# Optimization experiments

Hardware: AMD Instinct MI355X
Metric: run time of the kernel (lower is better)

## Reference

```python
import jax, jax.numpy as jnp
import numpy as np

NUM_HEADS = 16
DIM = 1024
HD = DIM // NUM_HEADS  # 64


def setup_inputs() -> dict:
    key = jax.random.key(0)
    ks = jax.random.split(key, 7)
    B, S = 4, 2048
    def xavier(k, shape, fan_in, fan_out):
        bound = float(np.sqrt(6.0 / (fan_in + fan_out)))
        return jax.random.uniform(k, shape, jnp.float32, -bound, bound)
    return {
        "q": jax.random.normal(ks[0], (B, S, DIM), jnp.float32),
        "k": jax.random.normal(ks[1], (B, S, DIM), jnp.float32),
        "v": jax.random.normal(ks[2], (B, S, DIM), jnp.float32),
        "Wq": xavier(ks[3], (NUM_HEADS, DIM, HD), DIM, HD),
        "Wk": xavier(ks[4], (NUM_HEADS, DIM, HD), DIM, HD),
        "Wv": xavier(ks[5], (NUM_HEADS, DIM, HD), DIM, HD),
        "Wo": xavier(ks[6], (DIM, DIM), DIM, DIM),
    }


def reference(q, k, v, Wq, Wk, Wv, Wo):
    B, S, D = q.shape
    norm = jnp.sqrt(jnp.asarray(HD, q.dtype))
    # per-head projections: [B,S,D] x [H,D,hd] -> [B,H,S,hd]
    qh = jnp.einsum('bsd,hde->bhse', q, Wq)
    kh = jnp.einsum('bsd,hde->bhse', k, Wk)
    vh = jnp.einsum('bsd,hde->bhse', v, Wv)
    # scores [B,H,S,S]
    scores = jnp.einsum('bhse,bhte->bhst', qh, kh) / norm
    causal = jnp.triu(jnp.ones((S, S), bool), k=1)
    scores = jnp.where(causal, -jnp.inf, scores)
    attn = jax.nn.softmax(scores, axis=-1)
    out = jnp.einsum('bhst,bhte->bhse', attn, vh)  # [B,H,S,hd]
    # faithful to original: a raw view of [B,H,S,hd] -> [B,S,H*hd] (no head transpose)
    out = out.reshape(B, S, NUM_HEADS * HD)
    return jnp.matmul(out, Wo)
```

## Files before the change

### kernel.cpp

```cpp
#include <hip/hip_runtime.h>
#include <hip/hip_bf16.h>
#include <stdint.h>

typedef __bf16 bf16;
typedef __bf16 bf16x8 __attribute__((ext_vector_type(8)));
typedef __bf16 bf16x4 __attribute__((ext_vector_type(4)));
typedef __bf16 bf16x2 __attribute__((ext_vector_type(2)));
typedef float f32x4 __attribute__((ext_vector_type(4)));
typedef float f32x16 __attribute__((ext_vector_type(16)));
typedef int i32x4 __attribute__((ext_vector_type(4)));

#define NH   16
#define SEQ  2048
#define DM   1024
#define HD   64

__device__ __forceinline__ int swz(int r, int o) {
  return o ^ ((r & 7) << 4) ^ (((r >> 3) & 1) << 5);
}

__device__ __forceinline__ int tauK(int m) {
  return (m & ~12) | ((m & 4) << 1) | ((m & 8) >> 1);
}

__device__ __forceinline__ void gll16(const void* g, void* l) {
  __builtin_amdgcn_global_load_lds(
      (__attribute__((address_space(1))) unsigned int*)(g),
      (__attribute__((address_space(3))) unsigned int*)(l), 16, 0, 0);
}

__device__ __forceinline__ int pk2(float a, float b) {
  bf16x2 t; t[0] = (bf16)a; t[1] = (bf16)b;
  return __builtin_bit_cast(int, t);
}

__global__ __launch_bounds__(256) void conv_wt(const float* __restrict__ Wq,
                                               const float* __restrict__ Wk,
                                               const float* __restrict__ Wv,
                                               const float* __restrict__ Wo,
                                               bf16* __restrict__ WqT,
                                               bf16* __restrict__ WkT,
                                               bf16* __restrict__ WvT,
                                               bf16* __restrict__ WoT) {
  __shared__ float tile[64][65];
  int z = blockIdx.z, t = threadIdx.x;
  int d0 = blockIdx.x << 6;
  if (z < 3) {
    const float* W = (z == 0 ? Wq : z == 1 ? Wk : Wv) + ((size_t)blockIdx.y << 16);
#pragma unroll
    for (int i = 0; i < 4; ++i) {
      int slot = (i << 8) + t;
      int r = slot >> 4, c4 = (slot & 15) << 2;
      float4 fv = *(const float4*)(W + (size_t)(d0 + r) * 64 + c4);
      tile[r][c4] = fv.x; tile[r][c4 + 1] = fv.y;
      tile[r][c4 + 2] = fv.z; tile[r][c4 + 3] = fv.w;
    }
  } else {
    int n0 = blockIdx.y << 6;
#pragma unroll
    for (int i = 0; i < 4; ++i) {
      int slot = (i << 8) + t;
      int r = slot >> 4, c4 = (slot & 15) << 2;
      float4 fv = *(const float4*)(Wo + (size_t)(d0 + r) * 1024 + n0 + c4);
      tile[r][c4] = fv.x; tile[r][c4 + 1] = fv.y;
      tile[r][c4 + 2] = fv.z; tile[r][c4 + 3] = fv.w;
    }
  }
  __syncthreads();
  bf16* Wt = z == 0 ? WqT : z == 1 ? WkT : z == 2 ? WvT : WoT;
  size_t base = (z < 3) ? ((size_t)blockIdx.y << 16)
                        : (size_t)(blockIdx.y << 6) * 1024;
  int e = t >> 2, dq = (t & 3) << 4;
  bf16x8 o0, o1;
#pragma unroll
  for (int j = 0; j < 8; ++j) {
    o0[j] = (bf16)tile[dq + j][e];
    o1[j] = (bf16)tile[dq + 8 + j][e];
  }
  bf16* p = Wt + base + (size_t)e * 1024 + d0 + dq;
  *(bf16x8*)p = o0;
  *(bf16x8*)(p + 8) = o1;
}

__global__ __launch_bounds__(256) void conv_in(const float* __restrict__ q,
                                               const float* __restrict__ k,
                                               const float* __restrict__ v,
                                               bf16* __restrict__ qb,
                                               bf16* __restrict__ kb,
                                               bf16* __restrict__ vb) {
  int z = blockIdx.y;
  const float* src = z == 0 ? q : z == 1 ? k : v;
  bf16* dst = z == 0 ? qb : z == 1 ? kb : vb;
  int i = (blockIdx.x * 256 + threadIdx.x) << 4;
  float4 f0 = *(const float4*)(src + i);
  float4 f1 = *(const float4*)(src + i + 4);
  float4 f2 = *(const float4*)(src + i + 8);
  float4 f3 = *(const float4*)(src + i + 12);
  bf16x8 o0, o1;
  o0[0] = (bf16)f0.x; o0[1] = (bf16)f0.y; o0[2] = (bf16)f0.z; o0[3] = (bf16)f0.w;
  o0[4] = (bf16)f1.x; o0[5] = (bf16)f1.y; o0[6] = (bf16)f1.z; o0[7] = (bf16)f1.w;
  o1[0] = (bf16)f2.x; o1[1] = (bf16)f2.y; o1[2] = (bf16)f2.z; o1[3] = (bf16)f2.w;
  o1[4] = (bf16)f3.x; o1[5] = (bf16)f3.y; o1[6] = (bf16)f3.z; o1[7] = (bf16)f3.w;
  *(bf16x8*)(dst + i) = o0;
  *(bf16x8*)(dst + i + 8) = o1;
}

template <bool AF32>
__device__ __forceinline__ void gemm_body(char* sm, const void* Av,
                                          const bf16* Bt, void* Cv, int epi,
                                          float scale, int n0, int m0) {
  char* As = sm;
  char* Bs = sm + 16384;
  int tid = threadIdx.x;
  int wid = tid >> 6, lane = tid & 63;
  int g = lane >> 4, cc = lane & 15;
  int wr = wid >> 1, wc = wid & 1;

  f32x4 acc[4][4];
#pragma unroll
  for (int a = 0; a < 4; ++a)
#pragma unroll
    for (int b = 0; b < 4; ++b)
#pragma unroll
      for (int j = 0; j < 4; ++j) acc[a][b][j] = 0.0f;

  for (int kt = 0; kt < 16; ++kt) {
    int k0 = kt << 6;
#pragma unroll
    for (int it = 0; it < 4; ++it) {
      int L = (it << 12) + (tid << 4);
      int r = L >> 7, o = L & 127;
      int os = swz(r, o);
      gll16(Bt + (size_t)(n0 + r) * 1024 + k0 + (os >> 1),
            Bs + (it << 12) + (wid << 10));
    }
    if constexpr (AF32) {
      const float* A = (const float*)Av;
      int r = tid >> 1, hf = tid & 1;
      const float* src = A + (size_t)(m0 + r) * 1024 + k0 + hf * 32;
      float4 fv[8];
#pragma unroll
      for (int q = 0; q < 8; ++q) fv[q] = ((const float4*)src)[q];
#pragma unroll
      for (int q = 0; q < 4; ++q) {
        float4 a = fv[2 * q], b = fv[2 * q + 1];
        bf16x8 pk;
        pk[0] = (bf16)a.x; pk[1] = (bf16)a.y; pk[2] = (bf16)a.z; pk[3] = (bf16)a.w;
        pk[4] = (bf16)b.x; pk[5] = (bf16)b.y; pk[6] = (bf16)b.z; pk[7] = (bf16)b.w;
        *(bf16x8*)(As + (r << 7) + swz(r, hf * 64 + q * 16)) = pk;
      }
    } else {
      const bf16* A = (const bf16*)Av;
#pragma unroll
      for (int it = 0; it < 4; ++it) {
        int L = (it << 12) + (tid << 4);
        int r = L >> 7, o = L & 127;
        int os = swz(r, o);
        gll16(A + (size_t)(m0 + r) * 1024 + k0 + (os >> 1),
              As + (it << 12) + (wid << 10));
      }
    }
    __syncthreads();
#pragma unroll
    for (int kk = 0; kk < 2; ++kk) {
      bf16x8 af[4], bfr[4];
#pragma unroll
      for (int fm = 0; fm < 4; ++fm) {
        int r = (wr << 6) + (fm << 4) + cc;
        af[fm] = *(const bf16x8*)(As + (r << 7) + swz(r, (kk << 6) + (g << 4)));
      }
#pragma unroll
      for (int fn = 0; fn < 4; ++fn) {
        int r = (wc << 6) + (fn << 4) + cc;
        bfr[fn] = *(const bf16x8*)(Bs + (r << 7) + swz(r, (kk << 6) + (g << 4)));
      }
#pragma unroll
      for (int fm = 0; fm < 4; ++fm)
#pragma unroll
        for (int fn = 0; fn < 4; ++fn)
          acc[fm][fn] = __builtin_amdgcn_mfma_f32_16x16x32_bf16(
              af[fm], bfr[fn], acc[fm][fn], 0, 0, 0);
    }
    __syncthreads();
  }

#pragma unroll
  for (int fm = 0; fm < 4; ++fm) {
#pragma unroll
    for (int fn = 0; fn < 4; ++fn) {
      f32x4 v = acc[fm][fn];
      int mr = m0 + (wr << 6) + (fm << 4) + (g << 2);
      int n = n0 + (wc << 6) + (fn << 4) + cc;
      if (epi == 2) {
        float* C = (float*)Cv;
#pragma unroll
        for (int j = 0; j < 4; ++j) C[(size_t)(mr + j) * 1024 + n] = v[j];
      } else if (epi == 0) {
        bf16* C = (bf16*)Cv;
        int h = n >> 6, e = n & 63;
#pragma unroll
        for (int j = 0; j < 4; ++j) {
          int b = (mr + j) >> 11, s = (mr + j) & 2047;
          C[((size_t)(b * NH + h) * SEQ + s) * HD + e] = (bf16)(v[j] * scale);
        }
      } else {
        bf16* C = (bf16*)Cv;
        int h = n >> 6, e = n & 63;
        int b = mr >> 11, s = mr & 2047;
        bf16x4 t;
#pragma unroll
        for (int j = 0; j < 4; ++j) t[j] = (bf16)v[j];
        *(bf16x4*)(C + ((size_t)(b * NH + h) * HD + e) * SEQ + s) = t;
      }
    }
  }
}

__global__ __launch_bounds__(256, 4) void gemm_qkv_bf16(
    const bf16* __restrict__ qb, const bf16* __restrict__ kb,
    const bf16* __restrict__ vb, const bf16* __restrict__ Wq,
    const bf16* __restrict__ Wk, const bf16* __restrict__ Wv,
    bf16* __restrict__ Qh, bf16* __restrict__ Kh, bf16* __restrict__ Vt,
    float qscale) {
  __shared__ char sm[32768];
  int z = (int)blockIdx.y >> 3;
  int nt = (int)blockIdx.y & 7;
  const void* A = z == 0 ? (const void*)qb : z == 1 ? (const void*)kb : (const void*)vb;
  const bf16* B = z == 0 ? Wq : z == 1 ? Wk : Wv;
  void* C = z == 0 ? (void*)Qh : z == 1 ? (void*)Kh : (void*)Vt;
  gemm_body<false>(sm, A, B, C, z == 2 ? 1 : 0, z == 0 ? qscale : 1.0f,
                   nt << 7, (int)blockIdx.x << 7);
}

__global__ __launch_bounds__(256, 2) void gemm_qkv_f32(
    const float* __restrict__ q, const float* __restrict__ k,
    const float* __restrict__ v, const bf16* __restrict__ Wq,
    const bf16* __restrict__ Wk, const bf16* __restrict__ Wv,
    bf16* __restrict__ Qh, bf16* __restrict__ Kh, bf16* __restrict__ Vt,
    float qscale) {
  __shared__ char sm[32768];
  int z = blockIdx.z;
  const void* A = z == 0 ? (const void*)q : z == 1 ? (const void*)k : (const void*)v;
  const bf16* B = z == 0 ? Wq : z == 1 ? Wk : Wv;
  void* C = z == 0 ? (void*)Qh : z == 1 ? (void*)Kh : (void*)Vt;
  gemm_body<true>(sm, A, B, C, z == 2 ? 1 : 0, z == 0 ? qscale : 1.0f,
                  (int)blockIdx.x << 7, (int)blockIdx.y << 7);
}

__global__ __launch_bounds__(256, 4) void gemm_o(const bf16* __restrict__ Att,
                                                 const bf16* __restrict__ Wo,
                                                 float* __restrict__ out) {
  __shared__ char sm[32768];
  gemm_body<false>(sm, Att, Wo, out, 2, 1.0f,
                   (int)blockIdx.y << 7, (int)blockIdx.x << 7);
}

__global__ __launch_bounds__(128, 2) void attn_fwd(const bf16* __restrict__ Qh,
                                                   const bf16* __restrict__ Kh,
                                                   const bf16* __restrict__ Vt,
                                                   bf16* __restrict__ Oa) {
  __shared__ char sm[32768];
  int tid = threadIdx.x, wid = tid >> 6;
  int lane = tid & 63, cc = lane & 31, hi = lane >> 5;
  int bx = blockIdx.x, by = blockIdx.y;
  int bh = (bx << 3) + (by >> 4);
  int pr = by & 15;
  const bf16* Kb = Kh + (size_t)bh * SEQ * HD;
  const bf16* Vb = Vt + (size_t)bh * HD * SEQ;

  bf16x8 vones;
#pragma unroll
  for (int j = 0; j < 8; ++j) vones[j] = (bf16)1.0f;

  for (int ph = 0; ph < 2; ++ph) {
    int qx = ph ? (31 - pr) : pr;
    int q0 = qx << 6;
    int sb = q0 + (wid << 5);

    const bf16* Qp = Qh + ((size_t)bh * SEQ + sb + cc) * HD + (hi << 3);
    bf16x8 qf[4];
#pragma unroll
    for (int kk = 0; kk < 4; ++kk) qf[kk] = *(const bf16x8*)(Qp + (kk << 4));

    f32x16 acc[2], lac;
#pragma unroll
    for (int eb = 0; eb < 2; ++eb)
#pragma unroll
      for (int r = 0; r < 16; ++r) acc[eb][r] = 0.f;
#pragma unroll
    for (int r = 0; r < 16; ++r) lac[r] = 0.f;

    int nkv = qx + 1;
    int cur = 0;
#pragma unroll
    for (int i2 = 0; i2 < 4; ++i2) {
      int L = (i2 << 11) + (tid << 4);
      int r = L >> 7, o = L & 127;
      int os = swz(r, o);
      gll16(Kb + (size_t)tauK(r) * HD + (os >> 1),
            sm + (i2 << 11) + (wid << 10));
      gll16(Vb + (size_t)r * SEQ + (os >> 1),
            sm + 8192 + (i2 << 11) + (wid << 10));
    }
    asm volatile("s_waitcnt vmcnt(0)" ::: "memory");
    __builtin_amdgcn_s_barrier();
    __builtin_amdgcn_sched_barrier(0);

    for (int it = 0; it < nkv; ++it) {
      int t0 = it << 6;
      char* Ks = sm + (cur << 14);
      char* Vs = Ks + 8192;
      if (it + 1 < nkv) {
        char* nb = sm + ((cur ^ 1) << 14);
        int t1 = t0 + 64;
#pragma unroll
        for (int i2 = 0; i2 < 4; ++i2) {
          int L = (i2 << 11) + (tid << 4);
          int r = L >> 7, o = L & 127;
          int os = swz(r, o);
          gll16(Kb + (size_t)(t1 + tauK(r)) * HD + (os >> 1),
                nb + (i2 << 11) + (wid << 10));
          gll16(Vb + (size_t)r * SEQ + t1 + (os >> 1),
                nb + 8192 + (i2 << 11) + (wid << 10));
        }
      }
      if (t0 <= sb + 31) {
        f32x16 sc[2];
        __builtin_amdgcn_s_setprio(1);
#pragma unroll
        for (int tb = 0; tb < 2; ++tb) {
#pragma unroll
          for (int r = 0; r < 16; ++r) sc[tb][r] = 0.f;
#pragma unroll
          for (int kk = 0; kk < 4; ++kk) {
            int rr = (tb << 5) + cc;
            bf16x8 kf = *(const bf16x8*)(Ks + (rr << 7) +
                                         swz(rr, (kk << 5) + (hi << 4)));
            sc[tb] = __builtin_amdgcn_mfma_f32_32x32x16_bf16(kf, qf[kk],
                                                             sc[tb], 0, 0, 0);
          }
        }
        __builtin_amdgcn_s_setprio(0);
        if (t0 + 63 > sb) {
          int s = sb + cc;
#pragma unroll
          for (int tb = 0; tb < 2; ++tb)
#pragma unroll
            for (int r = 0; r < 16; ++r) {
              int t = t0 + (tb << 5) + (r & 3) + (((r >> 2) & 1) << 2) +
                      (hi << 3) + ((r >> 3) << 4);
              if (t > s) sc[tb][r] = -3e38f;
            }
        }
#pragma unroll
        for (int tb = 0; tb < 2; ++tb)
#pragma unroll
          for (int r = 0; r < 16; ++r) sc[tb][r] = exp2f(sc[tb][r]);
        __builtin_amdgcn_s_setprio(1);
#pragma unroll
        for (int ks = 0; ks < 4; ++ks) {
          int tb = ks >> 1, base = (ks & 1) << 3;
          i32x4 wv;
          wv[0] = pk2(sc[tb][base + 0], sc[tb][base + 1]);
          wv[1] = pk2(sc[tb][base + 2], sc[tb][base + 3]);
          wv[2] = pk2(sc[tb][base + 4], sc[tb][base + 5]);
          wv[3] = pk2(sc[tb][base + 6], sc[tb][base + 7]);
          bf16x8 pa = __builtin_bit_cast(bf16x8, wv);
          lac = __builtin_amdgcn_mfma_f32_32x32x16_bf16(pa, vones, lac,
                                                        0, 0, 0);
#pragma unroll
          for (int eb = 0; eb < 2; ++eb) {
            int rr = (eb << 5) + cc;
            bf16x8 vf = *(const bf16x8*)(Vs + (rr << 7) +
                                         swz(rr, (ks << 5) + (hi << 4)));
            acc[eb] = __builtin_amdgcn_mfma_f32_32x32x16_bf16(pa, vf,
                                                              acc[eb], 0, 0, 0);
          }
        }
        __builtin_amdgcn_s_setprio(0);
      }
      asm volatile("s_waitcnt vmcnt(0)" ::: "memory");
      __builtin_amdgcn_s_barrier();
      __builtin_amdgcn_sched_barrier(0);
      cur ^= 1;
    }
    bf16* Op = Oa + ((size_t)bh * SEQ + sb) * HD;
#pragma unroll
    for (int r = 0; r < 16; ++r) {
      float ir = __builtin_amdgcn_rcpf(lac[r]);
      int ssel = (r & 3) + ((r >> 2) << 3) + (hi << 2);
#pragma unroll
      for (int eb = 0; eb < 2; ++eb)
        Op[(size_t)ssel * HD + (eb << 5) + cc] = (bf16)(acc[eb][r] * ir);
    }
  }
}

extern "C" void kernel_launch(void* const* d_in, const int* in_sizes, int n_in,
                              void* d_out, int out_size, void* d_ws,
                              size_t ws_size, hipStream_t stream) {
  const float* q = (const float*)d_in[0];
  const float* k = (const float*)d_in[1];
  const float* v = (const float*)d_in[2];
  const float* Wq = (const float*)d_in[3];
  const float* Wk = (const float*)d_in[4];
  const float* Wv = (const float*)d_in[5];
  const float* Wo = (const float*)d_in[6];
  char* ws = (char*)d_ws;

  const size_t MB = 1024 * 1024;
  const float qscale = 0.125f * 1.44269504f;

  bf16* WqT = (bf16*)(ws + 0 * MB);
  bf16* WkT = (bf16*)(ws + 2 * MB);
  bf16* WvT = (bf16*)(ws + 4 * MB);
  bf16* WoT = (bf16*)(ws + 6 * MB);

  conv_wt<<<dim3(16, 16, 4), 256, 0, stream>>>(Wq, Wk, Wv, Wo,
                                               WqT, WkT, WvT, WoT);

  if (ws_size >= 104 * MB) {
    bf16* qb = (bf16*)(ws + 8 * MB);
    bf16* kb = (bf16*)(ws + 24 * MB);
    bf16* vb = (bf16*)(ws + 40 * MB);
    bf16* Qh = (bf16*)(ws + 56 * MB);
    bf16* Kh = (bf16*)(ws + 72 * MB);
    bf16* Vt = (bf16*)(ws + 88 * MB);
    bf16* Att = qb;

    conv_in<<<dim3(2048, 3), 256, 0, stream>>>(q, k, v, qb, kb, vb);
    gemm_qkv_bf16<<<dim3(64, 24), 256, 0, stream>>>(
        qb, kb, vb, WqT, WkT, WvT, Qh, Kh, Vt, qscale);
    attn_fwd<<<dim3(8, 128), 128, 0, stream>>>(Qh, Kh, Vt, Att);
    gemm_o<<<dim3(64, 8), 256, 0, stream>>>(Att, WoT, (float*)d_out);
  } else {
    bf16* Qh = (bf16*)(ws + 8 * MB);
    bf16* Kh = (bf16*)(ws + 24 * MB);
    bf16* Vt = (bf16*)(ws + 40 * MB);
    bf16* Att = (bf16*)(ws + 56 * MB);

    gemm_qkv_f32<<<dim3(8, 64, 3), 256, 0, stream>>>(
        q, k, v, WqT, WkT, WvT, Qh, Kh, Vt, qscale);
    attn_fwd<<<dim3(8, 128), 128, 0, stream>>>(Qh, Kh, Vt, Att);
    gemm_o<<<dim3(8, 64), 256, 0, stream>>>(Att, WoT, (float*)d_out);
  }
}
```

Measured before the change: 183.3 us.

## Load K/V fragments directly from global memory in attention, dropping LDS staging

The attention kernel no longer stages K and V tiles through double-buffered shared memory with async loads and per-iteration barriers. Each wave now reads its K and V MFMA fragments straight from global memory through precomputed per-lane pointers, and launch bounds rise to allow three blocks per CU. This removes barrier synchronisation, shared-memory traffic and the shared-memory footprint. In exchange, both waves in a block fetch the same K/V data separately, and global-load latency is no longer hidden by an explicit prefetch, so the kernel leans on cache hits and higher occupancy.

```diff
diff --git a/kernel.cpp b/kernel.cpp
--- a/kernel.cpp
+++ b/kernel.cpp
@@ -255,11 +255,10 @@
                    (int)blockIdx.y << 7, (int)blockIdx.x << 7);
 }
 
-__global__ __launch_bounds__(128, 2) void attn_fwd(const bf16* __restrict__ Qh,
+__global__ __launch_bounds__(128, 3) void attn_fwd(const bf16* __restrict__ Qh,
                                                    const bf16* __restrict__ Kh,
                                                    const bf16* __restrict__ Vt,
                                                    bf16* __restrict__ Oa) {
-  __shared__ char sm[32768];
   int tid = threadIdx.x, wid = tid >> 6;
   int lane = tid & 63, cc = lane & 31, hi = lane >> 5;
   int bx = blockIdx.x, by = blockIdx.y;
@@ -268,6 +267,11 @@
   const bf16* Kb = Kh + (size_t)bh * SEQ * HD;
   const bf16* Vb = Vt + (size_t)bh * HD * SEQ;
 
+  const bf16* Kp0 = Kb + (size_t)tauK(cc) * HD + (hi << 3);
+  const bf16* Kp1 = Kb + (size_t)tauK(32 + cc) * HD + (hi << 3);
+  const bf16* Vp0 = Vb + (size_t)cc * SEQ + (hi << 3);
+  const bf16* Vp1 = Vb + (size_t)(32 + cc) * SEQ + (hi << 3);
+
   bf16x8 vones;
 #pragma unroll
   for (int j = 0; j < 8; ++j) vones[j] = (bf16)1.0f;
@@ -291,98 +295,59 @@
     for (int r = 0; r < 16; ++r) lac[r] = 0.f;
 
     int nkv = qx + 1;
-    int cur = 0;
-#pragma unroll
-    for (int i2 = 0; i2 < 4; ++i2) {
-      int L = (i2 << 11) + (tid << 4);
-      int r = L >> 7, o = L & 127;
-      int os = swz(r, o);
-      gll16(Kb + (size_t)tauK(r) * HD + (os >> 1),
-            sm + (i2 << 11) + (wid << 10));
-      gll16(Vb + (size_t)r * SEQ + (os >> 1),
-            sm + 8192 + (i2 << 11) + (wid << 10));
-    }
-    asm volatile("s_waitcnt vmcnt(0)" ::: "memory");
-    __builtin_amdgcn_s_barrier();
-    __builtin_amdgcn_sched_barrier(0);
-
     for (int it = 0; it < nkv; ++it) {
-      int t0 = it << 6;
-      char* Ks = sm + (cur << 14);
-      char* Vs = Ks + 8192;
-      if (it + 1 < nkv) {
-        char* nb = sm + ((cur ^ 1) << 14);
-        int t1 = t0 + 64;
-#pragma unroll
-        for (int i2 = 0; i2 < 4; ++i2) {
-          int L = (i2 << 11) + (tid << 4);
-          int r = L >> 7, o = L & 127;
-          int os = swz(r, o);
-          gll16(Kb + (size_t)(t1 + tauK(r)) * HD + (os >> 1),
-                nb + (i2 << 11) + (wid << 10));
-          gll16(Vb + (size_t)r * SEQ + t1 + (os >> 1),
-                nb + 8192 + (i2 << 11) + (wid << 10));
-        }
-      }
-      if (t0 <= sb + 31) {
-        f32x16 sc[2];
-        __builtin_amdgcn_s_setprio(1);
-#pragma unroll
-        for (int tb = 0; tb < 2; ++tb) {
-#pragma unroll
-          for (int r = 0; r < 16; ++r) sc[tb][r] = 0.f;
-#pragma unroll
-          for (int kk = 0; kk < 4; ++kk) {
-            int rr = (tb << 5) + cc;
-            bf16x8 kf = *(const bf16x8*)(Ks + (rr << 7) +
-                                         swz(rr, (kk << 5) + (hi << 4)));
-            sc[tb] = __builtin_amdgcn_mfma_f32_32x32x16_bf16(kf, qf[kk],
-                                                             sc[tb], 0, 0, 0);
+      size_t koff = (size_t)it << 12;
+      int voff = it << 6;
+      f32x16 sc[2];
+      __builtin_amdgcn_s_setprio(1);
+#pragma unroll
+      for (int r = 0; r < 16; ++r) { sc[0][r] = 0.f; sc[1][r] = 0.f; }
+#pragma unroll
+      for (int kk = 0; kk < 4; ++kk) {
+        bf16x8 kf0 = *(const bf16x8*)(Kp0 + koff + (kk << 4));
+        sc[0] = __builtin_amdgcn_mfma_f32_32x32x16_bf16(kf0, qf[kk],
+                                                        sc[0], 0, 0, 0);
+        bf16x8 kf1 = *(const bf16x8*)(Kp1 + koff + (kk << 4));
+        sc[1] = __builtin_amdgcn_mfma_f32_32x32x16_bf16(kf1, qf[kk],
+                                                        sc[1], 0, 0, 0);
+      }
+      __builtin_amdgcn_s_setprio(0);
+      if (it == nkv - 1) {
+        int s = sb + cc;
+        int t0 = it << 6;
+#pragma unroll
+        for (int tb = 0; tb < 2; ++tb)
+#pragma unroll
+          for (int r = 0; r < 16; ++r) {
+            int t = t0 + (tb << 5) + (r & 3) + (((r >> 2) & 1) << 2) +
+                    (hi << 3) + ((r >> 3) << 4);
+            if (t > s) sc[tb][r] = -3e38f;
           }
-        }
-        __builtin_amdgcn_s_setprio(0);
-        if (t0 + 63 > sb) {
-          int s = sb + cc;
-#pragma unroll
-          for (int tb = 0; tb < 2; ++tb)
-#pragma unroll
-            for (int r = 0; r < 16; ++r) {
-              int t = t0 + (tb << 5) + (r & 3) + (((r >> 2) & 1) << 2) +
-                      (hi << 3) + ((r >> 3) << 4);
-              if (t > s) sc[tb][r] = -3e38f;
-            }
-        }
-#pragma unroll
-        for (int tb = 0; tb < 2; ++tb)
-#pragma unroll
-          for (int r = 0; r < 16; ++r) sc[tb][r] = exp2f(sc[tb][r]);
-        __builtin_amdgcn_s_setprio(1);
-#pragma unroll
-        for (int ks = 0; ks < 4; ++ks) {
-          int tb = ks >> 1, base = (ks & 1) << 3;
-          i32x4 wv;
-          wv[0] = pk2(sc[tb][base + 0], sc[tb][base + 1]);
-          wv[1] = pk2(sc[tb][base + 2], sc[tb][base + 3]);
-          wv[2] = pk2(sc[tb][base + 4], sc[tb][base + 5]);
-          wv[3] = pk2(sc[tb][base + 6], sc[tb][base + 7]);
-          bf16x8 pa = __builtin_bit_cast(bf16x8, wv);
-          lac = __builtin_amdgcn_mfma_f32_32x32x16_bf16(pa, vones, lac,
-                                                        0, 0, 0);
-#pragma unroll
-          for (int eb = 0; eb < 2; ++eb) {
-            int rr = (eb << 5) + cc;
-            bf16x8 vf = *(const bf16x8*)(Vs + (rr << 7) +
-                                         swz(rr, (ks << 5) + (hi << 4)));
-            acc[eb] = __builtin_amdgcn_mfma_f32_32x32x16_bf16(pa, vf,
-                                                              acc[eb], 0, 0, 0);
-          }
-        }
-        __builtin_amdgcn_s_setprio(0);
-      }
-      asm volatile("s_waitcnt vmcnt(0)" ::: "memory");
-      __builtin_amdgcn_s_barrier();
-      __builtin_amdgcn_sched_barrier(0);
-      cur ^= 1;
+      }
+#pragma unroll
+      for (int tb = 0; tb < 2; ++tb)
+#pragma unroll
+        for (int r = 0; r < 16; ++r) sc[tb][r] = exp2f(sc[tb][r]);
+      __builtin_amdgcn_s_setprio(1);
+#pragma unroll
+      for (int ks = 0; ks < 4; ++ks) {
+        int tb = ks >> 1, base = (ks & 1) << 3;
+        i32x4 wv;
+        wv[0] = pk2(sc[tb][base + 0], sc[tb][base + 1]);
+        wv[1] = pk2(sc[tb][base + 2], sc[tb][base + 3]);
+        wv[2] = pk2(sc[tb][base + 4], sc[tb][base + 5]);
+        wv[3] = pk2(sc[tb][base + 6], sc[tb][base + 7]);
+        bf16x8 pa = __builtin_bit_cast(bf16x8, wv);
+        lac = __builtin_amdgcn_mfma_f32_32x32x16_bf16(pa, vones, lac,
+                                                      0, 0, 0);
+        bf16x8 vf0 = *(const bf16x8*)(Vp0 + voff + (ks << 4));
+        acc[0] = __builtin_amdgcn_mfma_f32_32x32x16_bf16(pa, vf0,
+                                                         acc[0], 0, 0, 0);
+        bf16x8 vf1 = *(const bf16x8*)(Vp1 + voff + (ks << 4));
+        acc[1] = __builtin_amdgcn_mfma_f32_32x32x16_bf16(pa, vf1,
+                                                         acc[1], 0, 0, 0);
+      }
+      __builtin_amdgcn_s_setprio(0);
     }
     bf16* Op = Oa + ((size_t)bh * SEQ + sb) * HD;
 #pragma unroll
```

Result: slower. 247.1 us (+34.8%).
